# Kernel tuning notes

Hardware: AMD Instinct MI355X
Metric: run time of the kernel (lower is better)

Reference implementation:

```python
import jax, jax.numpy as jnp
import numpy as np

EPS = 1e-6
NUM_HEADS = 16


def rms_norm(x, w):
    # x: [..., D], normalize over last dim, learnable scale w [D]
    var = jnp.mean(jnp.square(x), axis=-1, keepdims=True)
    return x * jax.lax.rsqrt(var + EPS) * w


def setup_inputs() -> dict:
    key = jax.random.key(0)
    ks = jax.random.split(key, 6)
    B, N, C = 8, 1024, 1024
    return {
        "x": jax.random.normal(ks[0], (B, N, C), dtype=jnp.float32),
        "w_qkv": jax.random.normal(ks[1], (3 * C, C), dtype=jnp.float32) * (1.0 / np.sqrt(C)),
        "b_qkv": jax.random.normal(ks[2], (3 * C,), dtype=jnp.float32) * 0.02,
        "qn_w": jnp.ones((C // NUM_HEADS,), dtype=jnp.float32),
        "kn_w": jnp.ones((C // NUM_HEADS,), dtype=jnp.float32),
        "w_proj": jax.random.normal(ks[3], (C, C), dtype=jnp.float32) * (1.0 / np.sqrt(C)),
        "b_proj": jax.random.normal(ks[4], (C,), dtype=jnp.float32) * 0.02,
    }


def reference(x, w_qkv, b_qkv, qn_w, kn_w, w_proj, b_proj):
    B, N, C = x.shape
    H = NUM_HEADS
    D = C // H
    # QKV projection: [B,N,3C] -> [3,B,H,N,D]
    qkv = x @ w_qkv.T + b_qkv
    qkv = qkv.reshape(B, N, 3, H, D).transpose(2, 0, 3, 1, 4)
    q, k, v = qkv[0], qkv[1], qkv[2]
    q = rms_norm(q, qn_w)
    k = rms_norm(k, kn_w)
    # scaled dot-product attention (no mask, no dropout in eval)
    scale = 1.0 / np.sqrt(D).astype(np.float32)
    attn = jnp.einsum('bhld,bhsd->bhls', q, k) * scale  # [B,H,N,N]
    attn = jax.nn.softmax(attn, axis=-1)
    out = jnp.einsum('bhls,bhsd->bhld', attn, v)  # [B,H,N,D]
    out = out.transpose(0, 2, 1, 3).reshape(B, N, C)
    return out @ w_proj.T + b_proj
```

## Files before the change

kernel.cpp:

```cpp
#include <hip/hip_runtime.h>
#include <hip/hip_bf16.h>
#include <stdint.h>

#define M_ROWS 8192
#define C_DIM  1024
#define QKV_N  3072

typedef _Float16 f16;
typedef __attribute__((ext_vector_type(8))) _Float16 f16x8;
typedef __attribute__((ext_vector_type(8))) short short8_t;
typedef __attribute__((ext_vector_type(4))) float float4_t;
typedef unsigned short u16;
typedef unsigned int u32;

__device__ __forceinline__ u16 f16_bits(float x) {
  union { f16 h; u16 u; } c; c.h = (f16)x; return c.u;
}
__device__ __forceinline__ u16 f32_to_bf16(float f) {
  u32 u = __float_as_uint(f);
  u32 r = (u + 0x7fffu + ((u >> 16) & 1u)) >> 16;
  return (u16)r;
}
__device__ __forceinline__ float bf16_to_f32(u16 h) {
  return __uint_as_float((u32)h << 16);
}
__device__ __forceinline__ void gld_lds16(const void* g, void* l) {
  __builtin_amdgcn_global_load_lds(
      (const __attribute__((address_space(1))) u32*)g,
      (__attribute__((address_space(3))) u32*)l, 16, 0, 0);
}
__device__ __forceinline__ int elem_off(int row, int e0) {
  return row * 64 + (e0 ^ ((row & 7) << 3));
}

__global__ __launch_bounds__(256) void split_bf16(
    const float* __restrict__ in, u16* __restrict__ hi, u16* __restrict__ lo) {
  int i = blockIdx.x * 256 + threadIdx.x;
  float4 v = ((const float4*)in)[i];
  float x[4] = {v.x, v.y, v.z, v.w};
  union { u16 u[4]; uint2 v2; } H, L;
#pragma unroll
  for (int j = 0; j < 4; ++j) {
    u16 h = f32_to_bf16(x[j]);
    H.u[j] = h;
    L.u[j] = f32_to_bf16(x[j] - bf16_to_f32(h));
  }
  ((uint2*)hi)[i] = H.v2;
  ((uint2*)lo)[i] = L.v2;
}

template <int MODE>
__global__ __launch_bounds__(256) void gemm_split(
    const u16* __restrict__ Ah, const u16* __restrict__ Al,
    const u16* __restrict__ Bh, const u16* __restrict__ Bl,
    const float* __restrict__ bias, void* __restrict__ O0,
    void* __restrict__ O1, void* __restrict__ O2,
    const float* __restrict__ qn_w, const float* __restrict__ kn_w,
    int M, int N, int K) {
  __shared__ u16 sAh[128 * 32], sAl[128 * 32], sBh[128 * 32], sBl[128 * 32];
  const int t = threadIdx.x;
  const int wv = t >> 6;
  const int lane = t & 63;
  const int n0 = blockIdx.x * 128;
  const int m0 = blockIdx.y * 128;
  const int wm = wv >> 1, wn = wv & 1;
  const int fr = lane & 15;
  const int g = lane >> 4;
  const int kfr = g * 8;

  float4_t acc[4][4];
  const float4_t zero = {0.f, 0.f, 0.f, 0.f};
#pragma unroll
  for (int i = 0; i < 4; ++i)
#pragma unroll
    for (int j = 0; j < 4; ++j) acc[i][j] = zero;

  for (int k0 = 0; k0 < K; k0 += 32) {
#pragma unroll
    for (int u = 0; u < 2; ++u) {
      int idx = u * 256 + t;
      int row = idx >> 2;
      int ke = (idx & 3) * 8;
      int ldsoff = (u * 256 + wv * 64) * 8;
      const size_t ga = (size_t)(m0 + row) * K + k0 + ke;
      const size_t gb = (size_t)(n0 + row) * K + k0 + ke;
      gld_lds16(Ah + ga, sAh + ldsoff);
      gld_lds16(Al + ga, sAl + ldsoff);
      gld_lds16(Bh + gb, sBh + ldsoff);
      gld_lds16(Bl + gb, sBl + ldsoff);
    }
    __syncthreads();

    short8_t ah[4], al[4], bh[4], bl[4];
#pragma unroll
    for (int i = 0; i < 4; ++i) {
      ah[i] = *(const short8_t*)&sAh[(wm * 64 + i * 16 + fr) * 32 + kfr];
      al[i] = *(const short8_t*)&sAl[(wm * 64 + i * 16 + fr) * 32 + kfr];
      bh[i] = *(const short8_t*)&sBh[(wn * 64 + i * 16 + fr) * 32 + kfr];
      bl[i] = *(const short8_t*)&sBl[(wn * 64 + i * 16 + fr) * 32 + kfr];
    }
#pragma unroll
    for (int i = 0; i < 4; ++i)
#pragma unroll
      for (int j = 0; j < 4; ++j) {
        acc[i][j] = __builtin_amdgcn_mfma_f32_16x16x32_bf16(ah[i], bh[j], acc[i][j], 0, 0, 0);
        acc[i][j] = __builtin_amdgcn_mfma_f32_16x16x32_bf16(ah[i], bl[j], acc[i][j], 0, 0, 0);
        acc[i][j] = __builtin_amdgcn_mfma_f32_16x16x32_bf16(al[i], bh[j], acc[i][j], 0, 0, 0);
      }
    __syncthreads();
  }

  const int r0 = g * 4;
  const int nw = n0 + wn * 64;
  float bz[4];
#pragma unroll
  for (int j = 0; j < 4; ++j) bz[j] = bias[nw + j * 16 + fr];

  if (MODE == 0) {
    const int sec = nw >> 10;
    const int h = (nw >> 6) & 15;
    u16* O = (sec == 0) ? (u16*)O0 : ((sec == 1) ? (u16*)O1 : (u16*)O2);
    float wn_[4];
    if (sec < 2) {
      const float* wvec = (sec == 0) ? qn_w : kn_w;
#pragma unroll
      for (int j = 0; j < 4; ++j) wn_[j] = wvec[j * 16 + fr];
    }
#pragma unroll
    for (int i = 0; i < 4; ++i) {
      float val[4][4];
#pragma unroll
      for (int j = 0; j < 4; ++j)
#pragma unroll
        for (int r = 0; r < 4; ++r) val[j][r] = acc[i][j][r] + bz[j];
      if (sec < 2) {
#pragma unroll
        for (int r = 0; r < 4; ++r) {
          float ss = 0.f;
#pragma unroll
          for (int j = 0; j < 4; ++j) ss += val[j][r] * val[j][r];
#pragma unroll
          for (int mask = 8; mask >= 1; mask >>= 1) ss += __shfl_xor(ss, mask);
          float sc = rsqrtf(ss * (1.0f / 64.0f) + 1e-6f);
#pragma unroll
          for (int j = 0; j < 4; ++j) val[j][r] *= sc * wn_[j];
        }
      }
#pragma unroll
      for (int j = 0; j < 4; ++j) {
        int col = h * 64 + j * 16 + fr;
#pragma unroll
        for (int r = 0; r < 4; ++r) {
          int m = m0 + wm * 64 + i * 16 + r0 + r;
          O[(size_t)m * 1024 + col] = f16_bits(val[j][r]);
        }
      }
    }
  } else {
    float* O = (float*)O0;
#pragma unroll
    for (int j = 0; j < 4; ++j) {
      int n = nw + j * 16 + fr;
#pragma unroll
      for (int i = 0; i < 4; ++i) {
        int mb = m0 + wm * 64 + i * 16 + r0;
#pragma unroll
        for (int r = 0; r < 4; ++r)
          O[(size_t)(mb + r) * 1024 + n] = acc[i][j][r] + bz[j];
      }
    }
  }
}

__global__ __launch_bounds__(256) void vtrans16(const u16* __restrict__ v,
                                                u16* __restrict__ vt) {
  __shared__ __align__(16) u16 T[64][80];
  const int t = threadIdx.x;
  const int nb = blockIdx.x;
  const int bh = blockIdx.y;
  const int b = bh >> 4, h = bh & 15;
  const int n0 = nb * 64;
#pragma unroll
  for (int u = 0; u < 2; ++u) {
    int idx = u * 256 + t;
    int row = idx >> 3;
    int c8 = (idx & 7) * 8;
    uint4 val = *(const uint4*)&v[((size_t)(b * 1024 + n0 + row)) * 1024 + h * 64 + c8];
    *(uint4*)&T[row][c8] = val;
  }
  __syncthreads();
#pragma unroll
  for (int u = 0; u < 2; ++u) {
    int idx = u * 256 + t;
    int d = idx >> 3;
    int n8 = (idx & 7) * 8;
    union { u16 q[8]; uint4 v4; } P;
#pragma unroll
    for (int i = 0; i < 8; ++i) P.q[i] = T[n8 + i][d];
    *(uint4*)&vt[((size_t)bh * 64 + d) * 1024 + n0 + n8] = P.v4;
  }
}

__device__ __forceinline__ void stage_tile64_512(const u16* __restrict__ src,
                                                 u16* __restrict__ lds, int t,
                                                 int rowbase, size_t stride,
                                                 int colbase) {
  int row = t >> 3;
  int cs = (t & 7) ^ (row & 7);
  gld_lds16(src + (size_t)(rowbase + row) * stride + colbase + cs * 8,
            lds + (size_t)t * 8);
}

__global__ __launch_bounds__(512) void flash_f16(
    const u16* __restrict__ q, const u16* __restrict__ k,
    const u16* __restrict__ vt, u16* __restrict__ ao_hi,
    u16* __restrict__ ao_lo) {
  __shared__ __align__(16) u16 sK[2][4096];
  __shared__ __align__(16) u16 sV[2][4096];
  const int t = threadIdx.x;
  const int wv = t >> 6, lane = t & 63;
  const int fr = lane & 15;
  const int g = lane >> 4;
  int flat = blockIdx.x;
  int nf = (flat & 7) * 128 + (flat >> 3);
  const int qb = nf & 7, bh = nf >> 3;
  const int q0 = qb * 128;
  const int b = bh >> 4, h = bh & 15;

  const u16* qrow = q + ((size_t)(b * 1024 + q0 + wv * 16 + fr)) * 1024 + h * 64;
  const u16* krow = k + ((size_t)b * 1024) * 1024 + h * 64;
  const u16* vbase = vt + (size_t)bh * 64 * 1024;

  f16x8 aQ[2];
#pragma unroll
  for (int c = 0; c < 2; ++c)
    aQ[c] = *(const f16x8*)&qrow[c * 32 + g * 8];

  float m_run = -1e30f, l_run = 0.f;
  float4_t o[4];
  const float4_t zero = {0.f, 0.f, 0.f, 0.f};
#pragma unroll
  for (int dt = 0; dt < 4; ++dt) o[dt] = zero;
  const float scale = 0.125f;

  stage_tile64_512(krow, &sK[0][0], t, 0, 1024, 0);
  stage_tile64_512(vbase, &sV[0][0], t, 0, 1024, 0);
  __syncthreads();

  int cur = 0;
  for (int it = 0; it < 16; ++it) {
    const int k0 = it * 64;
    if (it < 15) {
      stage_tile64_512(krow, &sK[cur ^ 1][0], t, k0 + 64, 1024, 0);
      stage_tile64_512(vbase, &sV[cur ^ 1][0], t, 0, 1024, k0 + 64);
    }
    const u16* sKc = &sK[cur][0];
    const u16* sVc = &sV[cur][0];

    float4_t sac[4];
#pragma unroll
    for (int j = 0; j < 4; ++j) sac[j] = zero;
#pragma unroll
    for (int j = 0; j < 4; ++j) {
      f16x8 kb0 = *(const f16x8*)&sKc[elem_off(j * 16 + fr, g * 8)];
      f16x8 kb1 = *(const f16x8*)&sKc[elem_off(j * 16 + fr, 32 + g * 8)];
      __builtin_amdgcn_s_setprio(1);
      sac[j] = __builtin_amdgcn_mfma_f32_16x16x32_f16(kb0, aQ[0], sac[j], 0, 0, 0);
      sac[j] = __builtin_amdgcn_mfma_f32_16x16x32_f16(kb1, aQ[1], sac[j], 0, 0, 0);
      __builtin_amdgcn_s_setprio(0);
    }

    float sv[4][4];
    float pmax = -1e30f;
#pragma unroll
    for (int j = 0; j < 4; ++j)
#pragma unroll
      for (int r = 0; r < 4; ++r) {
        sv[j][r] = sac[j][r] * scale;
        pmax = fmaxf(pmax, sv[j][r]);
      }
    pmax = fmaxf(pmax, __shfl_xor(pmax, 16));
    pmax = fmaxf(pmax, __shfl_xor(pmax, 32));
    float m_new = fmaxf(m_run, pmax);
    float corr = __expf(m_run - m_new);
    float rs = 0.f;
    u32 pk[4][2];
#pragma unroll
    for (int j = 0; j < 4; ++j) {
      float p0 = __expf(sv[j][0] - m_new);
      float p1 = __expf(sv[j][1] - m_new);
      float p2 = __expf(sv[j][2] - m_new);
      float p3 = __expf(sv[j][3] - m_new);
      rs += (p0 + p1) + (p2 + p3);
      pk[j][0] = (u32)f16_bits(p0) | ((u32)f16_bits(p1) << 16);
      pk[j][1] = (u32)f16_bits(p2) | ((u32)f16_bits(p3) << 16);
    }
    rs += __shfl_xor(rs, 16);
    rs += __shfl_xor(rs, 32);
    l_run = fmaf(l_run, corr, rs);
    m_run = m_new;

#pragma unroll
    for (int r = 0; r < 4; ++r) {
      float cr = __shfl(corr, (lane & 48) + ((lane >> 4) << 2) + r);
#pragma unroll
      for (int dt = 0; dt < 4; ++dt) o[dt][r] *= cr;
    }

    const int s0 = fr + ((g & 1) << 5);
    const int s1 = s0 + 16;
    const bool hi = ((g >> 1) & 1) != 0;
    f16x8 pa[2];
#pragma unroll
    for (int c = 0; c < 2; ++c) {
      const int jA = 2 * c, jB = 2 * c + 1;
      u32 a0 = (u32)__shfl((int)pk[jA][0], s0);
      u32 a1 = (u32)__shfl((int)pk[jA][1], s0);
      u32 b0 = (u32)__shfl((int)pk[jB][0], s0);
      u32 b1 = (u32)__shfl((int)pk[jB][1], s0);
      u32 a2 = (u32)__shfl((int)pk[jA][0], s1);
      u32 a3 = (u32)__shfl((int)pk[jA][1], s1);
      u32 b2 = (u32)__shfl((int)pk[jB][0], s1);
      u32 b3 = (u32)__shfl((int)pk[jB][1], s1);
      union { u32 w[4]; f16x8 v; } U;
      U.w[0] = hi ? b0 : a0;
      U.w[1] = hi ? b1 : a1;
      U.w[2] = hi ? b2 : a2;
      U.w[3] = hi ? b3 : a3;
      pa[c] = U.v;
    }

#pragma unroll
    for (int dt = 0; dt < 4; ++dt) {
      f16x8 vb0 = *(const f16x8*)&sVc[elem_off(dt * 16 + fr, g * 8)];
      f16x8 vb1 = *(const f16x8*)&sVc[elem_off(dt * 16 + fr, 32 + g * 8)];
      __builtin_amdgcn_s_setprio(1);
      o[dt] = __builtin_amdgcn_mfma_f32_16x16x32_f16(pa[0], vb0, o[dt], 0, 0, 0);
      o[dt] = __builtin_amdgcn_mfma_f32_16x16x32_f16(pa[1], vb1, o[dt], 0, 0, 0);
      __builtin_amdgcn_s_setprio(0);
    }

    __syncthreads();
    cur ^= 1;
  }

#pragma unroll
  for (int r = 0; r < 4; ++r) {
    float lq = __shfl(l_run, (lane & 48) + ((lane >> 4) << 2) + r);
    float inv = 1.0f / lq;
    int qg = q0 + wv * 16 + g * 4 + r;
#pragma unroll
    for (int dt = 0; dt < 4; ++dt) {
      float v = o[dt][r] * inv;
      u16 hb = f32_to_bf16(v);
      size_t off = ((size_t)(b * 1024 + qg)) * 1024 + h * 64 + dt * 16 + fr;
      ao_hi[off] = hb;
      ao_lo[off] = f32_to_bf16(v - bf16_to_f32(hb));
    }
  }
}

extern "C" void kernel_launch(void* const* d_in, const int* in_sizes, int n_in,
                              void* d_out, int out_size, void* d_ws, size_t ws_size,
                              hipStream_t stream) {
  const float* x      = (const float*)d_in[0];
  const float* w_qkv  = (const float*)d_in[1];
  const float* b_qkv  = (const float*)d_in[2];
  const float* qn_w   = (const float*)d_in[3];
  const float* kn_w   = (const float*)d_in[4];
  const float* w_proj = (const float*)d_in[5];
  const float* b_proj = (const float*)d_in[6];
  float* out = (float*)d_out;

  u16* x_hi  = (u16*)d_ws;
  u16* x_lo  = x_hi + 8388608;
  u16* wq_hi = x_lo + 8388608;
  u16* wq_lo = wq_hi + 3145728;
  u16* wp_hi = wq_lo + 3145728;
  u16* wp_lo = wp_hi + 1048576;
  u16* qb    = wp_lo + 1048576;
  u16* kb    = qb + 8388608;
  u16* vb    = kb + 8388608;
  u16* vtb   = vb + 8388608;
  u16* ao_hi = vtb + 8388608;
  u16* ao_lo = ao_hi + 8388608;

  split_bf16<<<8192, 256, 0, stream>>>(x, x_hi, x_lo);
  split_bf16<<<3072, 256, 0, stream>>>(w_qkv, wq_hi, wq_lo);
  split_bf16<<<1024, 256, 0, stream>>>(w_proj, wp_hi, wp_lo);

  gemm_split<0><<<dim3(QKV_N / 128, M_ROWS / 128), 256, 0, stream>>>(
      x_hi, x_lo, wq_hi, wq_lo, b_qkv, qb, kb, vb, qn_w, kn_w,
      M_ROWS, QKV_N, C_DIM);

  vtrans16<<<dim3(16, 128), 256, 0, stream>>>(vb, vtb);

  flash_f16<<<1024, 512, 0, stream>>>(qb, kb, vtb, ao_hi, ao_lo);

  gemm_split<1><<<dim3(C_DIM / 128, M_ROWS / 128), 256, 0, stream>>>(
      ao_hi, ao_lo, wp_hi, wp_lo, b_proj, out, nullptr, nullptr,
      nullptr, nullptr, M_ROWS, C_DIM, C_DIM);
}
```

Measured before the change: 401.6 us.

## Double-buffer LDS tiles in split-bf16 GEMM to overlap global loads with MFMA

Turns the single-buffered shared-memory staging in the split-precision GEMM into a two-buffer ping-pong. The next K tile's direct-to-LDS loads are issued before computing the current tile, with partial vmcnt waits and raw barriers replacing __syncthreads. This hides global load latency behind the MFMA work, at the cost of doubling LDS use per block (which may reduce occupancy) and depending on the hand-counted vmcnt value being correct.

```diff
diff --git a/kernel.cpp b/kernel.cpp
--- a/kernel.cpp
+++ b/kernel.cpp
@@ -57,7 +57,7 @@
     void* __restrict__ O1, void* __restrict__ O2,
     const float* __restrict__ qn_w, const float* __restrict__ kn_w,
     int M, int N, int K) {
-  __shared__ u16 sAh[128 * 32], sAl[128 * 32], sBh[128 * 32], sBl[128 * 32];
+  __shared__ u16 sAh[2 * 4096], sAl[2 * 4096], sBh[2 * 4096], sBl[2 * 4096];
   const int t = threadIdx.x;
   const int wv = t >> 6;
   const int lane = t & 63;
@@ -75,13 +75,13 @@
 #pragma unroll
     for (int j = 0; j < 4; ++j) acc[i][j] = zero;
 
-  for (int k0 = 0; k0 < K; k0 += 32) {
+  auto stage = [&](int buf, int k0) {
 #pragma unroll
     for (int u = 0; u < 2; ++u) {
       int idx = u * 256 + t;
       int row = idx >> 2;
       int ke = (idx & 3) * 8;
-      int ldsoff = (u * 256 + wv * 64) * 8;
+      int ldsoff = buf * 4096 + (u * 256 + wv * 64) * 8;
       const size_t ga = (size_t)(m0 + row) * K + k0 + ke;
       const size_t gb = (size_t)(n0 + row) * K + k0 + ke;
       gld_lds16(Ah + ga, sAh + ldsoff);
@@ -89,15 +89,32 @@
       gld_lds16(Bh + gb, sBh + ldsoff);
       gld_lds16(Bl + gb, sBl + ldsoff);
     }
-    __syncthreads();
-
+  };
+
+  stage(0, 0);
+  int cur = 0;
+  const int KT = K >> 5;
+  for (int kt = 0; kt < KT; ++kt) {
+    if (kt + 1 < KT) {
+      stage(cur ^ 1, (kt + 1) << 5);
+      asm volatile("s_waitcnt vmcnt(8)" ::: "memory");
+    } else {
+      asm volatile("s_waitcnt vmcnt(0)" ::: "memory");
+    }
+    __builtin_amdgcn_s_barrier();
+    asm volatile("" ::: "memory");
+
+    const u16* pAh = sAh + cur * 4096;
+    const u16* pAl = sAl + cur * 4096;
+    const u16* pBh = sBh + cur * 4096;
+    const u16* pBl = sBl + cur * 4096;
     short8_t ah[4], al[4], bh[4], bl[4];
 #pragma unroll
     for (int i = 0; i < 4; ++i) {
-      ah[i] = *(const short8_t*)&sAh[(wm * 64 + i * 16 + fr) * 32 + kfr];
-      al[i] = *(const short8_t*)&sAl[(wm * 64 + i * 16 + fr) * 32 + kfr];
-      bh[i] = *(const short8_t*)&sBh[(wn * 64 + i * 16 + fr) * 32 + kfr];
-      bl[i] = *(const short8_t*)&sBl[(wn * 64 + i * 16 + fr) * 32 + kfr];
+      ah[i] = *(const short8_t*)&pAh[(wm * 64 + i * 16 + fr) * 32 + kfr];
+      al[i] = *(const short8_t*)&pAl[(wm * 64 + i * 16 + fr) * 32 + kfr];
+      bh[i] = *(const short8_t*)&pBh[(wn * 64 + i * 16 + fr) * 32 + kfr];
+      bl[i] = *(const short8_t*)&pBl[(wn * 64 + i * 16 + fr) * 32 + kfr];
     }
 #pragma unroll
     for (int i = 0; i < 4; ++i)
@@ -107,7 +124,9 @@
         acc[i][j] = __builtin_amdgcn_mfma_f32_16x16x32_bf16(ah[i], bl[j], acc[i][j], 0, 0, 0);
         acc[i][j] = __builtin_amdgcn_mfma_f32_16x16x32_bf16(al[i], bh[j], acc[i][j], 0, 0, 0);
       }
-    __syncthreads();
+    asm volatile("" ::: "memory");
+    __builtin_amdgcn_s_barrier();
+    cur ^= 1;
   }
 
   const int r0 = g * 4;
```

Result: faster. 390.7 us (-2.7%).
